# Kernel tuning notes

Hardware: AMD Instinct MI355X
Metric: run time of the kernel (lower is better)

Reference implementation:

```python
import jax, jax.numpy as jnp
import numpy as np


def setup_inputs() -> dict:
    key = jax.random.key(0)
    ks = jax.random.split(key, 9)
    B, S, E, H, D = 8, 1000, 1024, 16, 64
    sc = 0.02
    return {
        "x": jax.random.normal(ks[0], (B, S, E), dtype=jnp.float32),
        "wq": jax.random.normal(ks[1], (H, E, D), dtype=jnp.float32) * sc,
        "bq": jax.random.normal(ks[2], (H, D), dtype=jnp.float32) * sc,
        "wk": jax.random.normal(ks[3], (H, E, D), dtype=jnp.float32) * sc,
        "bk": jax.random.normal(ks[4], (H, D), dtype=jnp.float32) * sc,
        "wv": jax.random.normal(ks[5], (H, E, D), dtype=jnp.float32) * sc,
        "bv": jax.random.normal(ks[6], (H, D), dtype=jnp.float32) * sc,
        "wp": jax.random.normal(ks[7], (E, E), dtype=jnp.float32) * sc,
        "bp": jax.random.normal(ks[8], (E,), dtype=jnp.float32) * sc,
    }


def reference(x, wq, bq, wk, bk, wv, bv, wp, bp):
    B, S, E = x.shape
    H, _, D = wq.shape
    # per-head projections, all heads batched: [B,H,S,D]
    q = jnp.einsum('bse,hed->bhsd', x, wq) + bq[None, :, None, :]
    k = jnp.einsum('bse,hed->bhsd', x, wk) + bk[None, :, None, :]
    v = jnp.einsum('bse,hed->bhsd', x, wv) + bv[None, :, None, :]
    # NOTE: original scales by sqrt(seq_len), not sqrt(head_dim)
    scores = jnp.einsum('bhsd,bhtd->bhst', q, k) / jnp.asarray(S, x.dtype) ** 0.5
    causal = jnp.tril(jnp.ones((S, S), dtype=bool))  # mask[:S,:S] == 1 keeps
    scores = jnp.where(causal, scores, jnp.asarray(-jnp.inf, x.dtype))
    attn = jax.nn.softmax(scores, axis=-1)
    z = jnp.einsum('bhst,bhtd->bhsd', attn, v)
    # concat heads in head order -> [B,S,E]
    y = z.transpose(0, 2, 1, 3).reshape(B, S, E)
    # projection then exact GELU (dropout is identity at eval)
    return jax.nn.gelu(jnp.einsum('bse,ef->bsf', y, wp) + bp, approximate=False)
```

## Files before the change

kernel.cpp:

```cpp
#include <hip/hip_runtime.h>
#include <hip/hip_bf16.h>
#include <math.h>

constexpr int B_ = 8, S_ = 1000, E_ = 1024, H_ = 16, D_ = 64;
constexpr int M_ = B_ * S_;

using bf16x8 = __attribute__((ext_vector_type(8))) __bf16;
using u16x8  = __attribute__((ext_vector_type(8))) unsigned short;
using f32x4  = __attribute__((ext_vector_type(4))) float;

static __device__ __forceinline__ unsigned short f2bf(float f) {
    union { float f; unsigned u; } c; c.f = f;
    return (unsigned short)((c.u + 0x7FFF + ((c.u >> 16) & 1)) >> 16);
}
static __device__ __forceinline__ unsigned short f2bf_fast(float f) {
    union { float f; unsigned u; } c; c.f = f;
    return (unsigned short)((c.u + 0x8000) >> 16);
}
static __device__ __forceinline__ float bfr2f(unsigned short s) {
    union { unsigned u; float f; } c; c.u = ((unsigned)s) << 16;
    return c.f;
}

static __device__ __forceinline__ void gld16(const unsigned short* g, unsigned short* lds) {
    __builtin_amdgcn_global_load_lds(
        (__attribute__((address_space(1))) void*)(g),
        (__attribute__((address_space(3))) void*)(lds), 16, 0, 0);
}

__global__ __launch_bounds__(256) void cast_x_kernel(
    const float* __restrict__ x, unsigned short* __restrict__ xbf)
{
    const size_t i = ((size_t)blockIdx.x * 256 + threadIdx.x) * 4;
    float4 v = *(const float4*)(x + i);
    ushort4 o;
    o.x = f2bf(v.x); o.y = f2bf(v.y); o.z = f2bf(v.z); o.w = f2bf(v.w);
    *(ushort4*)(xbf + i) = o;
}

__global__ __launch_bounds__(256) void transpose_wqkv_kernel(
    const float* __restrict__ wq, const float* __restrict__ wk,
    const float* __restrict__ wv, unsigned short* __restrict__ WT)
{
    __shared__ unsigned short Ts[64 * 65];
    const int et = blockIdx.x, zh = blockIdx.y;
    const int z = zh >> 4, h = zh & 15;
    const float* src = (z == 0 ? wq : z == 1 ? wk : wv) + (size_t)h * E_ * D_;

    const int d = threadIdx.x & 63;
    const int e0 = threadIdx.x >> 6;
    #pragma unroll
    for (int p = 0; p < 16; ++p) {
        const int e = e0 + p * 4;
        Ts[d * 65 + e] = f2bf(src[(size_t)(et * 64 + e) * D_ + d]);
    }
    __syncthreads();
    const int e = threadIdx.x & 63;
    const int d0 = threadIdx.x >> 6;
    #pragma unroll
    for (int p = 0; p < 16; ++p) {
        const int dd = d0 + p * 4;
        WT[((size_t)zh * 64 + dd) * E_ + et * 64 + e] = Ts[dd * 65 + e];
    }
}

__global__ __launch_bounds__(256) void transpose_wp_kernel(
    const float* __restrict__ wp, unsigned short* __restrict__ wpT)
{
    __shared__ unsigned short Ts[64 * 65];
    const int et = blockIdx.x, ft = blockIdx.y;
    const int f = threadIdx.x & 63;
    const int e0 = threadIdx.x >> 6;
    #pragma unroll
    for (int p = 0; p < 16; ++p) {
        const int e = e0 + p * 4;
        Ts[f * 65 + e] = f2bf(wp[(size_t)(et * 64 + e) * E_ + ft * 64 + f]);
    }
    __syncthreads();
    const int e = threadIdx.x & 63;
    const int f0 = threadIdx.x >> 6;
    #pragma unroll
    for (int p = 0; p < 16; ++p) {
        const int ff = f0 + p * 4;
        wpT[((size_t)(ft * 64 + ff)) * E_ + et * 64 + e] = Ts[ff * 65 + e];
    }
}

__global__ __launch_bounds__(256) void transpose_v_kernel(
    const unsigned short* __restrict__ vb, unsigned short* __restrict__ vt)
{
    __shared__ unsigned short Ts[64 * 65];
    const int st = blockIdx.x, bh = blockIdx.y;
    const size_t ibase = (size_t)bh * S_ * D_;
    const size_t obase = (size_t)bh * D_ * S_;

    const int d = threadIdx.x & 63;
    const int s0 = threadIdx.x >> 6;
    #pragma unroll
    for (int p = 0; p < 16; ++p) {
        const int s = s0 + p * 4;
        const int srow = st * 64 + s;
        Ts[s * 65 + d] = (srow < S_) ? vb[ibase + (size_t)srow * D_ + d] : 0;
    }
    __syncthreads();
    const int s = threadIdx.x & 63;
    const int d0 = threadIdx.x >> 6;
    const int scol = st * 64 + s;
    if (scol < S_) {
        #pragma unroll
        for (int p = 0; p < 16; ++p) {
            const int dd = d0 + p * 4;
            vt[obase + (size_t)dd * S_ + scol] = Ts[s * 65 + dd];
        }
    }
}

__global__ __launch_bounds__(256) void qkv_mfma_kernel(
    const unsigned short* __restrict__ xbf, const unsigned short* __restrict__ WT,
    const float* __restrict__ bq, const float* __restrict__ bk,
    const float* __restrict__ bv,
    unsigned short* __restrict__ qb, unsigned short* __restrict__ kb,
    unsigned short* __restrict__ vb)
{
    __shared__ unsigned short As[128 * 64];
    __shared__ unsigned short Bs[128 * 64];

    const int tid  = threadIdx.x;
    const int wave = tid >> 6, lane = tid & 63;
    const int m16  = lane & 15, quad = lane >> 4;
    const int wm   = wave >> 1, wn = wave & 1;
    const int n0   = blockIdx.x * 128;
    const int m0   = blockIdx.y * 128;

    f32x4 acc[4][4];
    #pragma unroll
    for (int nf = 0; nf < 4; ++nf)
        #pragma unroll
        for (int mf = 0; mf < 4; ++mf)
            acc[nf][mf] = (f32x4){0.f, 0.f, 0.f, 0.f};

    const int lrow = lane >> 3;
    const int lcol = (lane & 7) << 3;

    int a_srow[4];
    #pragma unroll
    for (int j = 0; j < 4; ++j) {
        int r = m0 + (wave * 4 + j) * 8 + lrow;
        a_srow[j] = (r < M_) ? r : (M_ - 1);
    }

    for (int kk = 0; kk < E_; kk += 64) {
        __syncthreads();
        #pragma unroll
        for (int j = 0; j < 4; ++j) {
            const int i = wave * 4 + j;
            gld16(xbf + (size_t)a_srow[j] * E_ + kk + lcol, &As[i * 512]);
            gld16(WT + (size_t)(n0 + i * 8 + lrow) * E_ + kk + lcol, &Bs[i * 512]);
        }
        __syncthreads();

        #pragma unroll
        for (int kh = 0; kh < 2; ++kh) {
            const int ko = kh * 32 + quad * 8;
            bf16x8 af[4];
            #pragma unroll
            for (int mf = 0; mf < 4; ++mf)
                af[mf] = *(const bf16x8*)&As[(wm * 64 + mf * 16 + m16) * 64 + ko];
            #pragma unroll
            for (int nf = 0; nf < 4; ++nf) {
                const bf16x8 bfr = *(const bf16x8*)&Bs[(wn * 64 + nf * 16 + m16) * 64 + ko];
                #pragma unroll
                for (int mf = 0; mf < 4; ++mf)
                    acc[nf][mf] = __builtin_amdgcn_mfma_f32_16x16x32_bf16(
                        af[mf], bfr, acc[nf][mf], 0, 0, 0);
            }
        }
    }

    const int z = n0 >> 10;
    const int h = ((n0 >> 6) + wn) & 15;
    unsigned short* const ob = (z == 0) ? qb : (z == 1) ? kb : vb;
    const float* const bz    = (z == 0) ? bq : (z == 1) ? bk : bv;

    float biasv[4];
    #pragma unroll
    for (int nf = 0; nf < 4; ++nf)
        biasv[nf] = bz[h * D_ + nf * 16 + m16];

    #pragma unroll
    for (int mf = 0; mf < 4; ++mf)
        #pragma unroll
        for (int r = 0; r < 4; ++r) {
            const int row = m0 + wm * 64 + mf * 16 + quad * 4 + r;
            if (row < M_) {
                const int b = row / S_, s = row % S_;
                const size_t obase = (((size_t)b * H_ + h) * S_ + s) * D_ + m16;
                #pragma unroll
                for (int nf = 0; nf < 4; ++nf)
                    ob[obase + nf * 16] = f2bf(acc[nf][mf][r] + biasv[nf]);
            }
        }
}

__global__ __launch_bounds__(512) void attn_flash_kernel(
    const unsigned short* __restrict__ q, const unsigned short* __restrict__ k,
    const unsigned short* __restrict__ vt, unsigned short* __restrict__ ybf)
{
    constexpr int P_ = 72;
    __shared__ unsigned short QP[128 * P_];
    __shared__ unsigned short Ks[64 * P_];
    __shared__ unsigned short Vt[64 * P_];

    const int tid  = threadIdx.x;
    const int wave = tid >> 6, lane = tid & 63;
    const int m16  = lane & 15, quad = lane >> 4;
    const int jq = (int)gridDim.x - 1 - (int)blockIdx.x;
    const int h = blockIdx.y, b = blockIdx.z;
    const size_t bh  = ((size_t)b * H_ + h) * S_;
    const size_t vtb = ((size_t)b * H_ + h) * (size_t)D_ * S_;
    const float sl2e = 0.031622776601683794f * 1.4426950408889634f;

    const int c8 = (tid & 7) * 8;
    const int r0 = tid >> 3;

    #pragma unroll
    for (int rr = 0; rr < 128; rr += 64) {
        const int r = r0 + rr;
        const int srow = jq * 128 + r;
        u16x8 val = {0, 0, 0, 0, 0, 0, 0, 0};
        if (srow < S_) val = *(const u16x8*)(q + (bh + srow) * D_ + c8);
        u16x8 o;
        #pragma unroll
        for (int jj = 0; jj < 8; ++jj) o[jj] = f2bf_fast(bfr2f(val[jj]) * sl2e);
        *(u16x8*)&QP[r * P_ + c8] = o;
    }
    __syncthreads();

    const bf16x8 qa0 = *(const bf16x8*)&QP[(wave * 16 + m16) * P_ + quad * 8];
    const bf16x8 qa1 = *(const bf16x8*)&QP[(wave * 16 + m16) * P_ + 32 + quad * 8];

    f32x4 O[4] = {{0,0,0,0},{0,0,0,0},{0,0,0,0},{0,0,0,0}};
    float l_i[4] = {0.f, 0.f, 0.f, 0.f};

    const int qrow_base = jq * 128 + wave * 16 + quad * 4;
    const int nt = 2 * jq + 2;

    u16x8 kreg = *(const u16x8*)(k + (bh + r0) * D_ + c8);
    u16x8 vreg = *(const u16x8*)(vt + vtb + (size_t)r0 * S_ + c8);

    for (int tt = 0; tt < nt; ++tt) {
        const int t0 = tt * 64;
        __syncthreads();
        *(u16x8*)&Ks[r0 * P_ + c8] = kreg;
        *(u16x8*)&Vt[r0 * P_ + c8] = vreg;
        __syncthreads();

        if (tt + 1 < nt) {
            const int nt0 = t0 + 64;
            const int srow = nt0 + r0;
            u16x8 kv = {0,0,0,0,0,0,0,0}, vv = {0,0,0,0,0,0,0,0};
            if (srow < S_) kv = *(const u16x8*)(k + (bh + srow) * D_ + c8);
            if (nt0 + c8 < S_)
                vv = *(const u16x8*)(vt + vtb + (size_t)r0 * S_ + nt0 + c8);
            kreg = kv; vreg = vv;
        }

        f32x4 sc[4];
        __builtin_amdgcn_s_setprio(1);
        #pragma unroll
        for (int ts = 0; ts < 4; ++ts) {
            const bf16x8 kb0 = *(const bf16x8*)&Ks[(ts * 16 + m16) * P_ + quad * 8];
            const bf16x8 kb1 = *(const bf16x8*)&Ks[(ts * 16 + m16) * P_ + 32 + quad * 8];
            f32x4 a = {0.f, 0.f, 0.f, 0.f};
            a = __builtin_amdgcn_mfma_f32_16x16x32_bf16(qa0, kb0, a, 0, 0, 0);
            a = __builtin_amdgcn_mfma_f32_16x16x32_bf16(qa1, kb1, a, 0, 0, 0);
            sc[ts] = a;
        }
        __builtin_amdgcn_s_setprio(0);

        unsigned short* const pw = &QP[wave * (16 * P_)];
        if (tt >= nt - 2) {
            #pragma unroll
            for (int ts = 0; ts < 4; ++ts) {
                const int t = t0 + ts * 16 + m16;
                #pragma unroll
                for (int r = 0; r < 4; ++r) {
                    float p = __builtin_amdgcn_exp2f(sc[ts][r]);
                    p = (t <= qrow_base + r) ? p : 0.f;
                    pw[(quad * 4 + r) * P_ + ts * 16 + m16] = f2bf_fast(p);
                    l_i[r] += p;
                }
            }
        } else {
            #pragma unroll
            for (int ts = 0; ts < 4; ++ts)
                #pragma unroll
                for (int r = 0; r < 4; ++r) {
                    const float p = __builtin_amdgcn_exp2f(sc[ts][r]);
                    pw[(quad * 4 + r) * P_ + ts * 16 + m16] = f2bf_fast(p);
                    l_i[r] += p;
                }
        }

        const bf16x8 pa0 = *(const bf16x8*)&pw[m16 * P_ + quad * 8];
        const bf16x8 pa1 = *(const bf16x8*)&pw[m16 * P_ + 32 + quad * 8];
        __builtin_amdgcn_s_setprio(1);
        #pragma unroll
        for (int db = 0; db < 4; ++db) {
            const bf16x8 vb0 = *(const bf16x8*)&Vt[(db * 16 + m16) * P_ + quad * 8];
            const bf16x8 vb1 = *(const bf16x8*)&Vt[(db * 16 + m16) * P_ + 32 + quad * 8];
            O[db] = __builtin_amdgcn_mfma_f32_16x16x32_bf16(pa0, vb0, O[db], 0, 0, 0);
            O[db] = __builtin_amdgcn_mfma_f32_16x16x32_bf16(pa1, vb1, O[db], 0, 0, 0);
        }
        __builtin_amdgcn_s_setprio(0);
    }

    #pragma unroll
    for (int off = 1; off < 16; off <<= 1)
        #pragma unroll
        for (int r = 0; r < 4; ++r)
            l_i[r] += __shfl_xor(l_i[r], off, 64);

    #pragma unroll
    for (int r = 0; r < 4; ++r) {
        const int qrow = qrow_base + r;
        if (qrow < S_) {
            const float invl = 1.0f / l_i[r];
            #pragma unroll
            for (int db = 0; db < 4; ++db)
                ybf[((size_t)b * S_ + qrow) * E_ + h * D_ + db * 16 + m16] =
                    f2bf(O[db][r] * invl);
        }
    }
}

__global__ __launch_bounds__(256) void proj_mfma_kernel(
    const unsigned short* __restrict__ ybf, const unsigned short* __restrict__ wpT,
    const float* __restrict__ bp, float* __restrict__ out)
{
    __shared__ unsigned short As[128 * 64];
    __shared__ unsigned short Bs[128 * 64];

    const int tid = threadIdx.x;
    const int wave = tid >> 6, lane = tid & 63;
    const int m16 = lane & 15, quad = lane >> 4;
    const int wm = wave >> 1, wn = wave & 1;
    const int m0 = blockIdx.x * 128;
    const int n0 = blockIdx.y * 128;

    f32x4 acc[4][4];
    #pragma unroll
    for (int nf = 0; nf < 4; ++nf)
        #pragma unroll
        for (int mf = 0; mf < 4; ++mf)
            acc[nf][mf] = (f32x4){0.f, 0.f, 0.f, 0.f};

    const int lrow = lane >> 3;
    const int lcol = (lane & 7) << 3;

    int a_srow[4];
    #pragma unroll
    for (int j = 0; j < 4; ++j) {
        int r = m0 + (wave * 4 + j) * 8 + lrow;
        a_srow[j] = (r < M_) ? r : (M_ - 1);
    }

    for (int kk = 0; kk < E_; kk += 64) {
        __syncthreads();
        #pragma unroll
        for (int j = 0; j < 4; ++j) {
            const int i = wave * 4 + j;
            gld16(ybf + (size_t)a_srow[j] * E_ + kk + lcol, &As[i * 512]);
            gld16(wpT + (size_t)(n0 + i * 8 + lrow) * E_ + kk + lcol, &Bs[i * 512]);
        }
        __syncthreads();

        #pragma unroll
        for (int kh = 0; kh < 2; ++kh) {
            const int ko = kh * 32 + quad * 8;
            bf16x8 af[4];
            #pragma unroll
            for (int mf = 0; mf < 4; ++mf)
                af[mf] = *(const bf16x8*)&As[(wm * 64 + mf * 16 + m16) * 64 + ko];
            #pragma unroll
            for (int nf = 0; nf < 4; ++nf) {
                const bf16x8 bfr = *(const bf16x8*)&Bs[(wn * 64 + nf * 16 + m16) * 64 + ko];
                #pragma unroll
                for (int mf = 0; mf < 4; ++mf)
                    acc[nf][mf] = __builtin_amdgcn_mfma_f32_16x16x32_bf16(
                        af[mf], bfr, acc[nf][mf], 0, 0, 0);
            }
        }
    }

    float biasv[4];
    #pragma unroll
    for (int nf = 0; nf < 4; ++nf)
        biasv[nf] = bp[n0 + wn * 64 + nf * 16 + m16];

    #pragma unroll
    for (int mf = 0; mf < 4; ++mf)
        #pragma unroll
        for (int r = 0; r < 4; ++r) {
            const int row = m0 + wm * 64 + mf * 16 + quad * 4 + r;
            if (row < M_) {
                #pragma unroll
                for (int nf = 0; nf < 4; ++nf) {
                    const int col = n0 + wn * 64 + nf * 16 + m16;
                    const float t = acc[nf][mf][r] + biasv[nf];
                    const float g = 0.5f * t * (1.0f + erff(t * 0.70710678118654752f));
                    out[(size_t)row * E_ + col] = g;
                }
            }
        }
}

extern "C" void kernel_launch(void* const* d_in, const int* in_sizes, int n_in,
                              void* d_out, int out_size, void* d_ws, size_t ws_size,
                              hipStream_t stream)
{
    const float* x  = (const float*)d_in[0];
    const float* wq = (const float*)d_in[1];
    const float* bq = (const float*)d_in[2];
    const float* wk = (const float*)d_in[3];
    const float* bk = (const float*)d_in[4];
    const float* wv = (const float*)d_in[5];
    const float* bv = (const float*)d_in[6];
    const float* wp = (const float*)d_in[7];
    const float* bp = (const float*)d_in[8];
    float* out = (float*)d_out;

    const size_t nME = (size_t)M_ * E_;
    unsigned short* xbf = (unsigned short*)d_ws;
    unsigned short* WT  = xbf + nME;
    unsigned short* wpT = WT + 3145728;
    unsigned short* qb  = wpT + 1048576;
    unsigned short* kb  = qb + nME;
    unsigned short* vb  = kb + nME;
    unsigned short* ybf = vb + nME;
    unsigned short* vtr = ybf + nME;

    cast_x_kernel<<<dim3((unsigned)(nME / 1024)), 256, 0, stream>>>(x, xbf);
    transpose_wqkv_kernel<<<dim3(16, 48), 256, 0, stream>>>(wq, wk, wv, WT);
    transpose_wp_kernel<<<dim3(16, 16), 256, 0, stream>>>(wp, wpT);

    qkv_mfma_kernel<<<dim3(3072 / 128, (M_ + 127) / 128), 256, 0, stream>>>(
        xbf, WT, bq, bk, bv, qb, kb, vb);
    transpose_v_kernel<<<dim3(16, B_ * H_), 256, 0, stream>>>(vb, vtr);
    attn_flash_kernel<<<dim3((S_ + 127) / 128, H_, B_), 512, 0, stream>>>(
        qb, kb, vtr, ybf);
    proj_mfma_kernel<<<dim3((M_ + 127) / 128, E_ / 128), 256, 0, stream>>>(
        ybf, wpT, bp, out);
}
```

Measured before the change: 288.8 us.

## Fuse V transpose and Q scaling into QKV GEMM epilogue

The QKV GEMM epilogue now writes V directly in transposed [D,S] layout and pre-scales Q by the softmax scale times log2(e), so the separate transpose_v kernel goes away. The attention kernel loads Q into LDS with direct global-to-LDS copies and no per-element rescale, using an unpadded 64-wide stride. This saves one launch and a full read/write of V, but the transposed V stores are strided per element and the unpadded Q layout may cause LDS bank conflicts. Q now gets one bf16 rounding after scaling instead of two.

After: 291.6 us. No clear change (+1.0%).

```diff
diff --git a/kernel.cpp b/kernel.cpp
--- a/kernel.cpp
+++ b/kernel.cpp
@@ -86,41 +86,12 @@
     }
 }
 
-__global__ __launch_bounds__(256) void transpose_v_kernel(
-    const unsigned short* __restrict__ vb, unsigned short* __restrict__ vt)
-{
-    __shared__ unsigned short Ts[64 * 65];
-    const int st = blockIdx.x, bh = blockIdx.y;
-    const size_t ibase = (size_t)bh * S_ * D_;
-    const size_t obase = (size_t)bh * D_ * S_;
-
-    const int d = threadIdx.x & 63;
-    const int s0 = threadIdx.x >> 6;
-    #pragma unroll
-    for (int p = 0; p < 16; ++p) {
-        const int s = s0 + p * 4;
-        const int srow = st * 64 + s;
-        Ts[s * 65 + d] = (srow < S_) ? vb[ibase + (size_t)srow * D_ + d] : 0;
-    }
-    __syncthreads();
-    const int s = threadIdx.x & 63;
-    const int d0 = threadIdx.x >> 6;
-    const int scol = st * 64 + s;
-    if (scol < S_) {
-        #pragma unroll
-        for (int p = 0; p < 16; ++p) {
-            const int dd = d0 + p * 4;
-            vt[obase + (size_t)dd * S_ + scol] = Ts[s * 65 + dd];
-        }
-    }
-}
-
 __global__ __launch_bounds__(256) void qkv_mfma_kernel(
     const unsigned short* __restrict__ xbf, const unsigned short* __restrict__ WT,
     const float* __restrict__ bq, const float* __restrict__ bk,
     const float* __restrict__ bv,
     unsigned short* __restrict__ qb, unsigned short* __restrict__ kb,
-    unsigned short* __restrict__ vb)
+    unsigned short* __restrict__ vt)
 {
     __shared__ unsigned short As[128 * 64];
     __shared__ unsigned short Bs[128 * 64];
@@ -179,27 +150,53 @@
 
     const int z = n0 >> 10;
     const int h = ((n0 >> 6) + wn) & 15;
-    unsigned short* const ob = (z == 0) ? qb : (z == 1) ? kb : vb;
-    const float* const bz    = (z == 0) ? bq : (z == 1) ? bk : bv;
-
-    float biasv[4];
-    #pragma unroll
-    for (int nf = 0; nf < 4; ++nf)
-        biasv[nf] = bz[h * D_ + nf * 16 + m16];
-
-    #pragma unroll
-    for (int mf = 0; mf < 4; ++mf)
-        #pragma unroll
-        for (int r = 0; r < 4; ++r) {
-            const int row = m0 + wm * 64 + mf * 16 + quad * 4 + r;
-            if (row < M_) {
-                const int b = row / S_, s = row % S_;
-                const size_t obase = (((size_t)b * H_ + h) * S_ + s) * D_ + m16;
-                #pragma unroll
-                for (int nf = 0; nf < 4; ++nf)
-                    ob[obase + nf * 16] = f2bf(acc[nf][mf][r] + biasv[nf]);
-            }
-        }
+
+    if (z == 2) {
+        float biasv[4];
+        #pragma unroll
+        for (int nf = 0; nf < 4; ++nf)
+            biasv[nf] = bv[h * D_ + nf * 16 + m16];
+
+        #pragma unroll
+        for (int mf = 0; mf < 4; ++mf)
+            #pragma unroll
+            for (int r = 0; r < 4; ++r) {
+                const int row = m0 + wm * 64 + mf * 16 + quad * 4 + r;
+                if (row < M_) {
+                    const int b = row / S_, s = row % S_;
+                    const size_t vtb = ((size_t)b * H_ + h) * (size_t)(D_ * S_);
+                    #pragma unroll
+                    for (int nf = 0; nf < 4; ++nf)
+                        vt[vtb + (size_t)(nf * 16 + m16) * S_ + s] =
+                            f2bf(acc[nf][mf][r] + biasv[nf]);
+                }
+            }
+    } else {
+        const float qscale = (z == 0)
+            ? (0.031622776601683794f * 1.4426950408889634f) : 1.0f;
+        unsigned short* const ob = (z == 0) ? qb : kb;
+        const float* const bz    = (z == 0) ? bq : bk;
+
+        float biasv[4];
+        #pragma unroll
+        for (int nf = 0; nf < 4; ++nf)
+            biasv[nf] = bz[h * D_ + nf * 16 + m16];
+
+        #pragma unroll
+        for (int mf = 0; mf < 4; ++mf)
+            #pragma unroll
+            for (int r = 0; r < 4; ++r) {
+                const int row = m0 + wm * 64 + mf * 16 + quad * 4 + r;
+                if (row < M_) {
+                    const int b = row / S_, s = row % S_;
+                    const size_t obase = (((size_t)b * H_ + h) * S_ + s) * D_ + m16;
+                    #pragma unroll
+                    for (int nf = 0; nf < 4; ++nf)
+                        ob[obase + nf * 16] =
+                            f2bf((acc[nf][mf][r] + biasv[nf]) * qscale);
+                }
+            }
+    }
 }
 
 __global__ __launch_bounds__(512) void attn_flash_kernel(
@@ -207,7 +204,7 @@
     const unsigned short* __restrict__ vt, unsigned short* __restrict__ ybf)
 {
     constexpr int P_ = 72;
-    __shared__ unsigned short QP[128 * P_];
+    __shared__ unsigned short QP[9216];
     __shared__ unsigned short Ks[64 * P_];
     __shared__ unsigned short Vt[64 * P_];
 
@@ -218,26 +215,21 @@
     const int h = blockIdx.y, b = blockIdx.z;
     const size_t bh  = ((size_t)b * H_ + h) * S_;
     const size_t vtb = ((size_t)b * H_ + h) * (size_t)D_ * S_;
-    const float sl2e = 0.031622776601683794f * 1.4426950408889634f;
 
     const int c8 = (tid & 7) * 8;
     const int r0 = tid >> 3;
 
     #pragma unroll
-    for (int rr = 0; rr < 128; rr += 64) {
-        const int r = r0 + rr;
-        const int srow = jq * 128 + r;
-        u16x8 val = {0, 0, 0, 0, 0, 0, 0, 0};
-        if (srow < S_) val = *(const u16x8*)(q + (bh + srow) * D_ + c8);
-        u16x8 o;
-        #pragma unroll
-        for (int jj = 0; jj < 8; ++jj) o[jj] = f2bf_fast(bfr2f(val[jj]) * sl2e);
-        *(u16x8*)&QP[r * P_ + c8] = o;
+    for (int j = 0; j < 2; ++j) {
+        const int i = wave * 2 + j;
+        int srow = jq * 128 + i * 8 + (lane >> 3);
+        if (srow >= S_) srow = S_ - 1;
+        gld16(q + (bh + srow) * D_ + (lane & 7) * 8, &QP[i * 512]);
     }
     __syncthreads();
 
-    const bf16x8 qa0 = *(const bf16x8*)&QP[(wave * 16 + m16) * P_ + quad * 8];
-    const bf16x8 qa1 = *(const bf16x8*)&QP[(wave * 16 + m16) * P_ + 32 + quad * 8];
+    const bf16x8 qa0 = *(const bf16x8*)&QP[(wave * 16 + m16) * 64 + quad * 8];
+    const bf16x8 qa1 = *(const bf16x8*)&QP[(wave * 16 + m16) * 64 + 32 + quad * 8];
 
     f32x4 O[4] = {{0,0,0,0},{0,0,0,0},{0,0,0,0},{0,0,0,0}};
     float l_i[4] = {0.f, 0.f, 0.f, 0.f};
@@ -436,17 +428,15 @@
     unsigned short* wpT = WT + 3145728;
     unsigned short* qb  = wpT + 1048576;
     unsigned short* kb  = qb + nME;
-    unsigned short* vb  = kb + nME;
-    unsigned short* ybf = vb + nME;
-    unsigned short* vtr = ybf + nME;
+    unsigned short* vtr = kb + nME;
+    unsigned short* ybf = vtr + nME;
 
     cast_x_kernel<<<dim3((unsigned)(nME / 1024)), 256, 0, stream>>>(x, xbf);
     transpose_wqkv_kernel<<<dim3(16, 48), 256, 0, stream>>>(wq, wk, wv, WT);
     transpose_wp_kernel<<<dim3(16, 16), 256, 0, stream>>>(wp, wpT);
 
     qkv_mfma_kernel<<<dim3(3072 / 128, (M_ + 127) / 128), 256, 0, stream>>>(
-        xbf, WT, bq, bk, bv, qb, kb, vb);
-    transpose_v_kernel<<<dim3(16, B_ * H_), 256, 0, stream>>>(vb, vtr);
+        xbf, WT, bq, bk, bv, qb, kb, vtr);
     attn_flash_kernel<<<dim3((S_ + 127) / 128, H_, B_), 512, 0, stream>>>(
         qb, kb, vtr, ybf);
     proj_mfma_kernel<<<dim3((M_ + 127) / 128, E_ / 128), 256, 0, stream>>>(
```
